# Kernel tuning notes

Hardware: AMD Instinct MI355X
Metric: run time of the kernel (lower is better)

The kernel has to match this reference:

```python
import jax, jax.numpy as jnp
import numpy as np

F, H1, H2, K, L = 16, 64, 64, 8, 8          # n_features, hidden sizes, num_bins, num_layers
NBP = 3 * K + 1                              # num_bijector_params per feature
RMIN, RMAX = -10.0, 10.0
MIN_BIN, MIN_SLOPE = 1e-4, 1e-4              # distrax RationalQuadraticSpline defaults


def setup_inputs() -> dict:
    key = jax.random.key(0)
    ks = jax.random.split(key, 11)
    B = 131072
    return {
        "x": jax.random.normal(ks[0], (B, F), jnp.float32),
        "W0": jax.random.normal(ks[1], (L, F, F), jnp.float32) * 0.1,
        "b0": jax.random.normal(ks[2], (L, F), jnp.float32) * 0.01,
        "W1": jax.random.normal(ks[3], (L, F, H1), jnp.float32) * 0.1,
        "b1": jax.random.normal(ks[4], (L, H1), jnp.float32) * 0.01,
        "W2": jax.random.normal(ks[5], (L, H1, H2), jnp.float32) * 0.1,
        "b2": jax.random.normal(ks[6], (L, H2), jnp.float32) * 0.01,
        "Wout": jax.random.normal(ks[7], (L, H2, F * NBP), jnp.float32) * 0.05,
        "bout": jax.random.normal(ks[8], (L, F * NBP), jnp.float32) * 0.01,
        # scalar-affine coupling params; scale kept positive (init is ones in the module)
        "scale": jnp.exp(0.05 * jax.random.normal(ks[9], (L, F), jnp.float32)),
        "shift": jax.random.normal(ks[10], (L, F), jnp.float32) * 0.1,
    }


def _rq_spline_fwd(params, x):
    """distrax.RationalQuadraticSpline forward_and_log_det (elementwise).
    params: (B, F, 3K+1), x: (B, F) -> (y, log_det) each (B, F)."""
    uw, uh, ud = params[..., :K], params[..., K:2 * K], params[..., 2 * K:]
    total = RMAX - RMIN
    w = jax.nn.softmax(uw, axis=-1) * (total - K * MIN_BIN) + MIN_BIN   # bin widths
    h = jax.nn.softmax(uh, axis=-1) * (total - K * MIN_BIN) + MIN_BIN   # bin heights
    offset = float(np.log(np.expm1(1.0 - MIN_SLOPE)))                   # softplus(0+offset)=1
    d = jax.nn.softplus(ud + offset) + MIN_SLOPE                        # knot slopes (B,F,K+1)
    zeros = jnp.zeros(w.shape[:-1] + (1,), w.dtype)
    xpos = RMIN + jnp.concatenate([zeros, jnp.cumsum(w, -1)], -1)       # knot x (B,F,K+1)
    ypos = RMIN + jnp.concatenate([zeros, jnp.cumsum(h, -1)], -1)       # knot y (B,F,K+1)
    # per-element bin search
    idx = jnp.clip(jnp.sum((x[..., None] >= xpos).astype(jnp.int32), -1) - 1, 0, K - 1)
    take = lambda a: jnp.take_along_axis(a, idx[..., None], axis=-1)[..., 0]
    xk, xk1 = take(xpos[..., :-1]), take(xpos[..., 1:])
    yk, yk1 = take(ypos[..., :-1]), take(ypos[..., 1:])
    dk, dk1 = take(d[..., :-1]), take(d[..., 1:])
    bw = xk1 - xk
    bh = yk1 - yk
    s = bh / bw                                                          # bin slope
    z = jnp.clip((x - xk) / bw, 0.0, 1.0)
    z1m = 1.0 - z
    den = s + (dk1 + dk - 2.0 * s) * z * z1m
    y = yk + bh * (s * z * z + dk * z * z1m) / den
    num_ld = dk1 * z * z + 2.0 * s * z * z1m + dk * z1m * z1m
    ld = 2.0 * jnp.log(s) + jnp.log(num_ld) - 2.0 * jnp.log(den)
    outside = (x <= RMIN) | (x >= RMAX)                                  # identity outside range
    return jnp.where(outside, x, y), jnp.where(outside, 0.0, ld)


def reference(x, W0, b0, W1, b1, W2, b2, Wout, bout, scale, shift):
    """log_prob of Transformed(base, Inverse(Chain(layers))) == base.log_prob(Chain.fwd(x)) + fwd logdet."""
    B = x.shape[0]
    feat = jnp.arange(F)
    z = x
    logdet = jnp.zeros((B,), x.dtype)
    # distrax.Chain applies the last-appended layer first -> iterate layers in reverse;
    # within layer i: spline coupling (appended second) then scalar-affine coupling.
    for i in reversed(range(L)):
        mask = ((feat + i) % 2).astype(bool)        # True = pass-through / conditioner input
        mz = jnp.where(mask, z, 0.0)
        hid = jnp.tanh(mz @ W0[i] + b0[i])
        hid = jnp.tanh(hid @ W1[i] + b1[i])
        hid = hid @ W2[i] + b2[i]                   # last MLP layer is linear
        p = (hid @ Wout[i] + bout[i]).reshape(B, F, NBP)
        y, ld = _rq_spline_fwd(p, z)
        z = jnp.where(mask, z, y)
        logdet = logdet + jnp.sum(jnp.where(mask, 0.0, ld), axis=-1)
        # scalar affine coupling with all-False mask: transforms every feature
        z = z * scale[i] + shift[i]
        logdet = logdet + jnp.sum(jnp.log(jnp.abs(scale[i])))
    base_lp = -0.5 * jnp.sum(z * z, axis=-1) - 0.5 * F * float(np.log(2.0 * np.pi))
    return base_lp + logdet
```

## Files before the change

### kernel.cpp

```cpp
#include <hip/hip_runtime.h>
#include <math.h>

typedef _Float16 f16;
typedef _Float16 half8 __attribute__((ext_vector_type(8)));
typedef float f32x16 __attribute__((ext_vector_type(16)));

#define DEV __device__ __forceinline__

#define W1F_OFF 0
#define W2F_OFF 16384
#define WOF_OFF 81920
#define BOF_OFF 344064
#define SUMLOG_OFF 352256
#define W0S_OFF 352320
#define B0S_OFF 360512
#define B1S_OFF 361088
#define BOT_OFF 363136

#define H0_OFF    0
#define H0_STRIDE 48
#define H_OFF     12288
#define H_STRIDE  144
#define P_OFF     49152
#define P_STRIDE  116
#define LDS_BYTES 78848

DEV float frcp(float x){ return __builtin_amdgcn_rcpf(x); }

#if __has_builtin(__builtin_amdgcn_exp2f)
DEV float fexp2(float x){ return __builtin_amdgcn_exp2f(x); }
#else
DEV float fexp2(float x){ return exp2f(x); }
#endif
#if __has_builtin(__builtin_amdgcn_logf)
DEV float flog2(float x){ return __builtin_amdgcn_logf(x); }
#else
DEV float flog2(float x){ return log2f(x); }
#endif

#define LN2F    0.69314718056f
#define LOG2EF  1.4426950409f
#define TWOLOG2EF 2.8853900818f

DEV float ftanh2(float x){
  float e = fexp2(x);
  float r = frcp(e + 1.f);
  return fmaf(-2.f, r, 1.f);
}

DEV void rq_spline(const float p[25], float xv, float &y_out, float &ld_out)
{
  float ew[8]; float sw = 0.f;
#pragma unroll
  for (int k = 0; k < 8; ++k){ ew[k] = fexp2(p[k]); sw += ew[k]; }
  float rw = frcp(sw) * 19.9992f;

  float xpos[9];
  xpos[0] = -10.f;
#pragma unroll
  for (int k = 0; k < 8; ++k) xpos[k + 1] = xpos[k] + fmaf(ew[k], rw, 1e-4f);

  bool b[8];
  int idx = 0;
#pragma unroll
  for (int j = 1; j < 8; ++j){ b[j] = (xv >= xpos[j]); idx += b[j] ? 1 : 0; }

  float xk = xpos[0], ewk = ew[0];
#pragma unroll
  for (int j = 1; j < 8; ++j){
    xk  = b[j] ? xpos[j] : xk;
    ewk = b[j] ? ew[j]   : ewk;
  }
  float bw = fmaf(ewk, rw, 1e-4f);

  float eh[8]; float shs = 0.f;
#pragma unroll
  for (int k = 0; k < 8; ++k){ eh[k] = fexp2(p[8 + k]); shs += eh[k]; }
  float rh = frcp(shs) * 19.9992f;

  float S = 0.f, ehk = eh[0];
#pragma unroll
  for (int k = 1; k < 8; ++k){
    S   += b[k] ? eh[k - 1] : 0.f;
    ehk  = b[k] ? eh[k]     : ehk;
  }
  float yk = fmaf(S, rh, fmaf((float)idx, 1e-4f, -10.f));
  float bh = fmaf(ehk, rh, 1e-4f);

  float vA = p[16], vB = p[17];
#pragma unroll
  for (int j = 1; j < 8; ++j){
    vA = b[j] ? p[16 + j] : vA;
    vB = b[j] ? p[17 + j] : vB;
  }
  float tA = fmaxf(vA, 0.f) + flog2(1.f + fexp2(-fabsf(vA)));
  float dk  = fmaf(LN2F, tA, 1e-4f);
  float tB = fmaxf(vB, 0.f) + flog2(1.f + fexp2(-fabsf(vB)));
  float dk1 = fmaf(LN2F, tB, 1e-4f);

  float rbw = frcp(bw);
  float s   = bh * rbw;
  float zf  = fminf(fmaxf((xv - xk) * rbw, 0.f), 1.f);
  float z1  = 1.f - zf;
  float zz  = zf * zf, z01 = zf * z1;
  float den = s + (dk1 + dk - 2.f * s) * z01;
  float rden = frcp(den);
  float yv  = yk + bh * (s * zz + dk * z01) * rden;
  float num = dk1 * zz + 2.f * s * z01 + dk * z1 * z1;
  float ldv2 = flog2(s * s * num * rden * rden);

  bool outside = (xv <= -10.f) || (xv >= 10.f);
  y_out  = outside ? xv : yv;
  ld_out = outside ? 0.f : ldv2;
}

extern "C" __global__ void __launch_bounds__(256)
prep_kernel(const float* __restrict__ W0, const float* __restrict__ b0,
            const float* __restrict__ W1, const float* __restrict__ b1,
            const float* __restrict__ W2,
            const float* __restrict__ Wo, const float* __restrict__ bout,
            const float* __restrict__ scale, char* __restrict__ ws)
{
  int tid = blockIdx.x * 256 + threadIdx.x;
  if (tid < 1024){
    int fi = tid >> 6, lane = tid & 63;
    int l = fi >> 1, nt = fi & 1;
    int n = nt * 32 + (lane & 31), khi = lane >> 5;
    half8 h;
#pragma unroll
    for (int j = 0; j < 8; ++j){ int k = khi * 8 + j; h[j] = (f16)(W1[l * 1024 + k * 64 + n] * TWOLOG2EF); }
    *(half8*)(ws + W1F_OFF + fi * 1024 + lane * 16) = h;
  } else if (tid < 5120){
    int idx = tid - 1024;
    int fi = idx >> 6, lane = idx & 63;
    int l = fi >> 3, kt = (fi >> 1) & 3, nt = fi & 1;
    int n = nt * 32 + (lane & 31), khi = lane >> 5;
    half8 h;
#pragma unroll
    for (int j = 0; j < 8; ++j){ int k = kt * 16 + khi * 8 + j; h[j] = (f16)W2[l * 4096 + k * 64 + n]; }
    *(half8*)(ws + W2F_OFF + fi * 1024 + lane * 16) = h;
  } else if (tid < 21504){
    int idx = tid - 5120;
    int fi = idx >> 6, lane = idx & 63;
    int l = fi >> 5, u = (fi >> 2) & 7, kt = fi & 3;
    int f = (l & 1) + 2 * u;
    int c = lane & 31, khi = lane >> 5;
    half8 h;
#pragma unroll
    for (int j = 0; j < 8; ++j){
      int k = kt * 16 + khi * 8 + j;
      float v = (c < 25) ? Wo[l * 25600 + k * 400 + f * 25 + c] * LOG2EF : 0.f;
      h[j] = (f16)v;
    }
    *(half8*)(ws + WOF_OFF + fi * 1024 + lane * 16) = h;
  } else if (tid < 23552){
    int idx = tid - 21504;
    int l = idx >> 8, u = (idx >> 5) & 7, c = idx & 31;
    int f = (l & 1) + 2 * u;
    float v = 0.f;
    if (c < 25){
      v = bout[l * 400 + f * 25 + c];
      if (c >= 16) v += 0.54116666f;
      v *= LOG2EF;
    }
    ((float*)(ws + BOF_OFF))[idx] = v;
  } else if (tid == 23552){
    float acc = 0.f;
    for (int i = 0; i < 128; ++i) acc += logf(fabsf(scale[i]));
    *(float*)(ws + SUMLOG_OFF) = acc;
  } else if (tid < 25601){
    int idx = tid - 23553;
    ((float*)(ws + W0S_OFF))[idx] = W0[idx] * TWOLOG2EF;
  } else if (tid < 25729){
    int idx = tid - 25601;
    ((float*)(ws + B0S_OFF))[idx] = b0[idx] * TWOLOG2EF;
  } else if (tid < 26241){
    int idx = tid - 25729;
    ((float*)(ws + B1S_OFF))[idx] = b1[idx] * TWOLOG2EF;
  } else if (tid < 28289){
    int idx = tid - 26241;
    int l = idx >> 8, u = (idx >> 5) & 7, kh = (idx >> 4) & 1, i = idx & 15;
    int f = (l & 1) + 2 * u;
    int r = (i & 3) + 8 * (i >> 2) + 4 * kh;
    float v = 0.f;
    if (r < 25){
      v = bout[l * 400 + f * 25 + r];
      if (r >= 16) v += 0.54116666f;
      v *= LOG2EF;
    }
    ((float*)(ws + BOT_OFF))[idx] = v;
  }
}

DEV void load_botv(const char* __restrict__ ws, int l, int u, int khi,
                   float (&botv)[16])
{
  const float4* bp = (const float4*)(ws + BOT_OFF) + ((l * 8 + u) * 2 + khi) * 4;
#pragma unroll
  for (int q = 0; q < 4; ++q){
    float4 v = bp[q];
    botv[q * 4]     = v.x;
    botv[q * 4 + 1] = v.y;
    botv[q * 4 + 2] = v.z;
    botv[q * 4 + 3] = v.w;
  }
}

DEV void wout_feature(const half8 (&a2)[2][4], const half8 (&bfn)[4],
                      const float (&botv)[16], char* lds,
                      int wv, int ln31, int khi)
{
  f32x16 dp[2];
#pragma unroll
  for (int mt = 0; mt < 2; ++mt)
#pragma unroll
    for (int i = 0; i < 16; ++i) dp[mt][i] = botv[i];
#pragma unroll
  for (int kt = 0; kt < 4; ++kt)
#pragma unroll
    for (int mt = 0; mt < 2; ++mt)
      dp[mt] = __builtin_amdgcn_mfma_f32_32x32x16_f16(bfn[kt], a2[mt][kt], dp[mt], 0, 0, 0);
#pragma unroll
  for (int mt = 0; mt < 2; ++mt){
    int s = wv * 64 + mt * 32 + ln31;
    char* base = lds + P_OFF + s * P_STRIDE + khi * 16;
#pragma unroll
    for (int i = 0; i < 12; ++i){
      int rc = (i & 3) + 8 * (i >> 2);
      *(float*)(base + rc * 4) = dp[mt][i];
    }
    if (khi == 0)
      *(float*)(base + 24 * 4) = dp[mt][12];
  }
}

template<int PAR>
DEV void layer_mfma(int l,
                    const float* __restrict__ b2v,
                    const float* __restrict__ scv, const float* __restrict__ shv,
                    const char* __restrict__ ws, char* lds,
                    float (&z)[16], float &logdet,
                    int t, int lane, int wv, int ln31, int khi)
{
  const float* w0  = (const float*)(ws + W0S_OFF) + l * 256;
  const float* bb0 = (const float*)(ws + B0S_OFF) + l * 16;
  const int rowbase = khi * 4;

  const half8* W1F = (const half8*)(ws + W1F_OFF);
  const half8* W2F = (const half8*)(ws + W2F_OFF);
  half8 w1f[2];
#pragma unroll
  for (int nt = 0; nt < 2; ++nt) w1f[nt] = W1F[(l * 2 + nt) * 64 + lane];
  half8 w2f[8];
#pragma unroll
  for (int kt = 0; kt < 4; ++kt)
#pragma unroll
    for (int nt = 0; nt < 2; ++nt)
      w2f[kt * 2 + nt] = W2F[((l * 4 + kt) * 2 + nt) * 64 + lane];
  float bias1[2], bias2[2];
#pragma unroll
  for (int nt = 0; nt < 2; ++nt){
    bias1[nt] = ((const float*)(ws + B1S_OFF))[l * 64 + nt * 32 + ln31];
    bias2[nt] = b2v[l * 64 + nt * 32 + ln31];
  }

  float h0[16];
#pragma unroll
  for (int j = 0; j < 16; ++j) h0[j] = bb0[j];
#pragma unroll
  for (int u = 0; u < 8; ++u){
    const int f = (1 - PAR) + 2 * u;
    const float v = z[f];
#pragma unroll
    for (int j = 0; j < 16; ++j) h0[j] = fmaf(v, w0[f * 16 + j], h0[j]);
  }
  {
    half8 lo, hi;
#pragma unroll
    for (int j = 0; j < 8; ++j){ lo[j] = (f16)ftanh2(h0[j]); hi[j] = (f16)ftanh2(h0[8 + j]); }
    *(half8*)(lds + H0_OFF + t * H0_STRIDE)      = lo;
    *(half8*)(lds + H0_OFF + t * H0_STRIDE + 16) = hi;
  }

  half8 a0[2];
#pragma unroll
  for (int mt = 0; mt < 2; ++mt){
    int s = wv * 64 + mt * 32 + ln31;
    a0[mt] = *(const half8*)(lds + H0_OFF + s * H0_STRIDE + khi * 16);
  }
  f32x16 d1[2][2];
#pragma unroll
  for (int mt = 0; mt < 2; ++mt)
#pragma unroll
    for (int nt = 0; nt < 2; ++nt)
#pragma unroll
      for (int i = 0; i < 16; ++i) d1[mt][nt][i] = bias1[nt];
#pragma unroll
  for (int nt = 0; nt < 2; ++nt)
#pragma unroll
    for (int mt = 0; mt < 2; ++mt)
      d1[mt][nt] = __builtin_amdgcn_mfma_f32_32x32x16_f16(a0[mt], w1f[nt], d1[mt][nt], 0, 0, 0);
#pragma unroll
  for (int mt = 0; mt < 2; ++mt)
#pragma unroll
    for (int nt = 0; nt < 2; ++nt)
#pragma unroll
      for (int i = 0; i < 16; ++i){
        int row = (i & 3) + 8 * (i >> 2) + rowbase;
        int s = wv * 64 + mt * 32 + row;
        float v = ftanh2(d1[mt][nt][i]);
        *(f16*)(lds + H_OFF + s * H_STRIDE + (nt * 32 + ln31) * 2) = (f16)v;
      }

  half8 a1[2][4];
#pragma unroll
  for (int mt = 0; mt < 2; ++mt){
    int s = wv * 64 + mt * 32 + ln31;
#pragma unroll
    for (int kt = 0; kt < 4; ++kt)
      a1[mt][kt] = *(const half8*)(lds + H_OFF + s * H_STRIDE + kt * 32 + khi * 16);
  }
  f32x16 d2[2][2];
#pragma unroll
  for (int mt = 0; mt < 2; ++mt)
#pragma unroll
    for (int nt = 0; nt < 2; ++nt)
#pragma unroll
      for (int i = 0; i < 16; ++i) d2[mt][nt][i] = bias2[nt];
#pragma unroll
  for (int kt = 0; kt < 4; ++kt)
#pragma unroll
    for (int nt = 0; nt < 2; ++nt)
#pragma unroll
      for (int mt = 0; mt < 2; ++mt)
        d2[mt][nt] = __builtin_amdgcn_mfma_f32_32x32x16_f16(a1[mt][kt], w2f[kt * 2 + nt], d2[mt][nt], 0, 0, 0);

  const half8* WOF = (const half8*)(ws + WOF_OFF);
  half8 bfn[4];
#pragma unroll
  for (int kt = 0; kt < 4; ++kt) bfn[kt] = WOF[((l * 8 + 0) * 4 + kt) * 64 + lane];
  float botv[16];
  load_botv(ws, l, 0, khi, botv);

#pragma unroll
  for (int mt = 0; mt < 2; ++mt)
#pragma unroll
    for (int nt = 0; nt < 2; ++nt)
#pragma unroll
      for (int i = 0; i < 16; ++i){
        int row = (i & 3) + 8 * (i >> 2) + rowbase;
        int s = wv * 64 + mt * 32 + row;
        float v = d2[mt][nt][i];
        *(f16*)(lds + H_OFF + s * H_STRIDE + (nt * 32 + ln31) * 2) = (f16)v;
      }

  half8 a2[2][4];
#pragma unroll
  for (int mt = 0; mt < 2; ++mt){
    int s = wv * 64 + mt * 32 + ln31;
#pragma unroll
    for (int kt = 0; kt < 4; ++kt)
      a2[mt][kt] = *(const half8*)(lds + H_OFF + s * H_STRIDE + kt * 32 + khi * 16);
  }

  wout_feature(a2, bfn, botv, lds, wv, ln31, khi);
#pragma unroll
  for (int kt = 0; kt < 4; ++kt) bfn[kt] = WOF[((l * 8 + 1) * 4 + kt) * 64 + lane];
  load_botv(ws, l, 1, khi, botv);

#pragma unroll 1
  for (int u = 0; u < 8; ++u){
    float p[25];
#pragma unroll
    for (int j = 0; j < 25; ++j)
      p[j] = *(const float*)(lds + P_OFF + t * P_STRIDE + j * 4);

    if (u < 7){
      wout_feature(a2, bfn, botv, lds, wv, ln31, khi);
      if (u < 6){
#pragma unroll
        for (int kt = 0; kt < 4; ++kt) bfn[kt] = WOF[((l * 8 + u + 2) * 4 + kt) * 64 + lane];
        load_botv(ws, l, u + 2, khi, botv);
      }
    }

    const int f = PAR + 2 * u;
    float y, ld;
    rq_spline(p, z[f], y, ld);
    z[f] = y;
    logdet += ld;
  }

  const float* scp = scv + l * 16;
  const float* shp = shv + l * 16;
#pragma unroll
  for (int j = 0; j < 16; ++j)
    z[j] = fmaf(z[j], scp[j], shp[j]);
}

extern "C" __global__ void __launch_bounds__(256, 2)
flow_kernel(const float* __restrict__ x,
            const float* __restrict__ b2v,
            const float* __restrict__ scv, const float* __restrict__ shv,
            const char* __restrict__ ws, float* __restrict__ out, int B)
{
  extern __shared__ char lds[];
  const int t    = threadIdx.x;
  const int lane = t & 63;
  const int wv   = t >> 6;
  const int ln31 = lane & 31;
  const int khi  = lane >> 5;
  const int g    = blockIdx.x * 256 + t;

  float z[16];
  const float4* xv = reinterpret_cast<const float4*>(x + (size_t)g * 16);
  float4 a0 = xv[0], a1 = xv[1], a2 = xv[2], a3 = xv[3];
  z[0]=a0.x; z[1]=a0.y; z[2]=a0.z; z[3]=a0.w;
  z[4]=a1.x; z[5]=a1.y; z[6]=a1.z; z[7]=a1.w;
  z[8]=a2.x; z[9]=a2.y; z[10]=a2.z; z[11]=a2.w;
  z[12]=a3.x; z[13]=a3.y; z[14]=a3.z; z[15]=a3.w;

  float logdet = 0.f;
  for (int l = 7; l >= 0; --l){
    if (l & 1) layer_mfma<1>(l, b2v, scv, shv, ws, lds, z, logdet, t, lane, wv, ln31, khi);
    else       layer_mfma<0>(l, b2v, scv, shv, ws, lds, z, logdet, t, lane, wv, ln31, khi);
  }

  float sumlog = *(const float*)(ws + SUMLOG_OFF);
  float ss = 0.f;
#pragma unroll
  for (int j = 0; j < 16; ++j) ss = fmaf(z[j], z[j], ss);
  out[g] = fmaf(LN2F, logdet, -0.5f * ss - 14.7030165f + sumlog);
}

extern "C" void kernel_launch(void* const* d_in, const int* in_sizes, int n_in,
                              void* d_out, int out_size, void* d_ws, size_t ws_size,
                              hipStream_t stream)
{
  const float* x    = (const float*)d_in[0];
  const float* W0   = (const float*)d_in[1];
  const float* b0   = (const float*)d_in[2];
  const float* W1   = (const float*)d_in[3];
  const float* b1   = (const float*)d_in[4];
  const float* W2   = (const float*)d_in[5];
  const float* b2   = (const float*)d_in[6];
  const float* Wout = (const float*)d_in[7];
  const float* bout = (const float*)d_in[8];
  const float* scale= (const float*)d_in[9];
  const float* shift= (const float*)d_in[10];

  int B = in_sizes[0] / 16;

  hipLaunchKernelGGL(prep_kernel, dim3(111), dim3(256), 0, stream,
                     W0, b0, W1, b1, W2, Wout, bout, scale, (char*)d_ws);

  hipLaunchKernelGGL(flow_kernel, dim3(B / 256), dim3(256), LDS_BYTES, stream,
                     x, b2, scale, shift,
                     (const char*)d_ws, (float*)d_out, B);
}
```

Before: 192.0 us.

## Transpose hidden MFMAs, alias per-wave LDS arena, raise occupancy to three blocks

Swaps the MFMA operand order for the two hidden layers so outputs come out transposed, which lets tanh results be written to LDS as packed half4 stores instead of scalar f16 stores. Biases are pre-laid out in the transposed accumulator order by the prep kernel. The H0, H and P buffers are aliased inside one 12 KB per-wave arena, shrinking LDS from about 77 KB to 48 KB, and launch bounds are raised to three blocks per CU. The aim is fewer LDS store instructions and higher occupancy. The cost is tighter register pressure under the new launch bound and reliance on wave-private LDS reuse, which is only safe because each wave touches nothing but its own arena.

```diff
diff --git a/kernel.cpp b/kernel.cpp
--- a/kernel.cpp
+++ b/kernel.cpp
@@ -2,7 +2,9 @@
 #include <math.h>
 
 typedef _Float16 f16;
+typedef _Float16 half4 __attribute__((ext_vector_type(4)));
 typedef _Float16 half8 __attribute__((ext_vector_type(8)));
+typedef float f32x4  __attribute__((ext_vector_type(4)));
 typedef float f32x16 __attribute__((ext_vector_type(16)));
 
 #define DEV __device__ __forceinline__
@@ -10,7 +12,8 @@
 #define W1F_OFF 0
 #define W2F_OFF 16384
 #define WOF_OFF 81920
-#define BOF_OFF 344064
+#define B1T_OFF 344064
+#define B2T_OFF 346112
 #define SUMLOG_OFF 352256
 #define W0S_OFF 352320
 #define B0S_OFF 360512
@@ -19,11 +22,12 @@
 
 #define H0_OFF    0
 #define H0_STRIDE 48
-#define H_OFF     12288
+#define H_OFF     3072
 #define H_STRIDE  144
-#define P_OFF     49152
+#define P_OFF     0
 #define P_STRIDE  116
-#define LDS_BYTES 78848
+#define ARENA     12288
+#define LDS_BYTES (4 * ARENA)
 
 DEV float frcp(float x){ return __builtin_amdgcn_rcpf(x); }
 
@@ -117,7 +121,7 @@
 extern "C" __global__ void __launch_bounds__(256)
 prep_kernel(const float* __restrict__ W0, const float* __restrict__ b0,
             const float* __restrict__ W1, const float* __restrict__ b1,
-            const float* __restrict__ W2,
+            const float* __restrict__ W2, const float* __restrict__ b2,
             const float* __restrict__ Wo, const float* __restrict__ bout,
             const float* __restrict__ scale, char* __restrict__ ws)
 {
@@ -153,31 +157,27 @@
       h[j] = (f16)v;
     }
     *(half8*)(ws + WOF_OFF + fi * 1024 + lane * 16) = h;
-  } else if (tid < 23552){
+  } else if (tid < 22016){
     int idx = tid - 21504;
-    int l = idx >> 8, u = (idx >> 5) & 7, c = idx & 31;
-    int f = (l & 1) + 2 * u;
-    float v = 0.f;
-    if (c < 25){
-      v = bout[l * 400 + f * 25 + c];
-      if (c >= 16) v += 0.54116666f;
-      v *= LOG2EF;
-    }
-    ((float*)(ws + BOF_OFF))[idx] = v;
+    int l = idx >> 6, nt = (idx >> 5) & 1, kh = (idx >> 4) & 1, i = idx & 15;
+    int r = (i & 3) + 8 * (i >> 2) + 4 * kh;
+    ((float*)(ws + B1T_OFF))[idx] = b1[l * 64 + nt * 32 + r] * TWOLOG2EF;
+  } else if (tid < 22528){
+    int idx = tid - 22016;
+    int l = idx >> 6, nt = (idx >> 5) & 1, kh = (idx >> 4) & 1, i = idx & 15;
+    int r = (i & 3) + 8 * (i >> 2) + 4 * kh;
+    ((float*)(ws + B2T_OFF))[idx] = b2[l * 64 + nt * 32 + r];
   } else if (tid == 23552){
     float acc = 0.f;
     for (int i = 0; i < 128; ++i) acc += logf(fabsf(scale[i]));
     *(float*)(ws + SUMLOG_OFF) = acc;
-  } else if (tid < 25601){
+  } else if (tid > 23552 && tid < 25601){
     int idx = tid - 23553;
     ((float*)(ws + W0S_OFF))[idx] = W0[idx] * TWOLOG2EF;
-  } else if (tid < 25729){
+  } else if (tid >= 25601 && tid < 25729){
     int idx = tid - 25601;
     ((float*)(ws + B0S_OFF))[idx] = b0[idx] * TWOLOG2EF;
-  } else if (tid < 26241){
-    int idx = tid - 25729;
-    ((float*)(ws + B1S_OFF))[idx] = b1[idx] * TWOLOG2EF;
-  } else if (tid < 28289){
+  } else if (tid >= 26241 && tid < 28289){
     int idx = tid - 26241;
     int l = idx >> 8, u = (idx >> 5) & 7, kh = (idx >> 4) & 1, i = idx & 15;
     int f = (l & 1) + 2 * u;
@@ -195,20 +195,16 @@
 DEV void load_botv(const char* __restrict__ ws, int l, int u, int khi,
                    float (&botv)[16])
 {
-  const float4* bp = (const float4*)(ws + BOT_OFF) + ((l * 8 + u) * 2 + khi) * 4;
-#pragma unroll
-  for (int q = 0; q < 4; ++q){
-    float4 v = bp[q];
-    botv[q * 4]     = v.x;
-    botv[q * 4 + 1] = v.y;
-    botv[q * 4 + 2] = v.z;
-    botv[q * 4 + 3] = v.w;
+  const f32x4* bp = (const f32x4*)(ws + BOT_OFF) + ((l * 8 + u) * 2 + khi) * 4;
+  f32x4 q0 = bp[0], q1 = bp[1], q2 = bp[2], q3 = bp[3];
+#pragma unroll
+  for (int i = 0; i < 4; ++i){
+    botv[i] = q0[i]; botv[4 + i] = q1[i]; botv[8 + i] = q2[i]; botv[12 + i] = q3[i];
   }
 }
 
 DEV void wout_feature(const half8 (&a2)[2][4], const half8 (&bfn)[4],
-                      const float (&botv)[16], char* lds,
-                      int wv, int ln31, int khi)
+                      const float (&botv)[16], char* ldsw, int ln31, int khi)
 {
   f32x16 dp[2];
 #pragma unroll
@@ -222,29 +218,27 @@
       dp[mt] = __builtin_amdgcn_mfma_f32_32x32x16_f16(bfn[kt], a2[mt][kt], dp[mt], 0, 0, 0);
 #pragma unroll
   for (int mt = 0; mt < 2; ++mt){
-    int s = wv * 64 + mt * 32 + ln31;
-    char* base = lds + P_OFF + s * P_STRIDE + khi * 16;
+    int s = mt * 32 + ln31;
+    char* base = ldsw + P_OFF + s * P_STRIDE + khi * 16;
 #pragma unroll
     for (int i = 0; i < 12; ++i){
       int rc = (i & 3) + 8 * (i >> 2);
       *(float*)(base + rc * 4) = dp[mt][i];
     }
     if (khi == 0)
-      *(float*)(base + 24 * 4) = dp[mt][12];
+      *(float*)(base + 96) = dp[mt][12];
   }
 }
 
 template<int PAR>
 DEV void layer_mfma(int l,
-                    const float* __restrict__ b2v,
                     const float* __restrict__ scv, const float* __restrict__ shv,
-                    const char* __restrict__ ws, char* lds,
+                    const char* __restrict__ ws, char* ldsw,
                     float (&z)[16], float &logdet,
-                    int t, int lane, int wv, int ln31, int khi)
+                    int lane, int ln31, int khi)
 {
   const float* w0  = (const float*)(ws + W0S_OFF) + l * 256;
   const float* bb0 = (const float*)(ws + B0S_OFF) + l * 16;
-  const int rowbase = khi * 4;
 
   const half8* W1F = (const half8*)(ws + W1F_OFF);
   const half8* W2F = (const half8*)(ws + W2F_OFF);
@@ -257,12 +251,6 @@
 #pragma unroll
     for (int nt = 0; nt < 2; ++nt)
       w2f[kt * 2 + nt] = W2F[((l * 4 + kt) * 2 + nt) * 64 + lane];
-  float bias1[2], bias2[2];
-#pragma unroll
-  for (int nt = 0; nt < 2; ++nt){
-    bias1[nt] = ((const float*)(ws + B1S_OFF))[l * 64 + nt * 32 + ln31];
-    bias2[nt] = b2v[l * 64 + nt * 32 + ln31];
-  }
 
   float h0[16];
 #pragma unroll
@@ -278,62 +266,78 @@
     half8 lo, hi;
 #pragma unroll
     for (int j = 0; j < 8; ++j){ lo[j] = (f16)ftanh2(h0[j]); hi[j] = (f16)ftanh2(h0[8 + j]); }
-    *(half8*)(lds + H0_OFF + t * H0_STRIDE)      = lo;
-    *(half8*)(lds + H0_OFF + t * H0_STRIDE + 16) = hi;
+    *(half8*)(ldsw + H0_OFF + lane * H0_STRIDE)      = lo;
+    *(half8*)(ldsw + H0_OFF + lane * H0_STRIDE + 16) = hi;
   }
 
   half8 a0[2];
 #pragma unroll
-  for (int mt = 0; mt < 2; ++mt){
-    int s = wv * 64 + mt * 32 + ln31;
-    a0[mt] = *(const half8*)(lds + H0_OFF + s * H0_STRIDE + khi * 16);
-  }
-  f32x16 d1[2][2];
-#pragma unroll
   for (int mt = 0; mt < 2; ++mt)
+    a0[mt] = *(const half8*)(ldsw + H0_OFF + (mt * 32 + ln31) * H0_STRIDE + khi * 16);
+  f32x16 d1t[2][2];
+  {
+    const f32x4* B1T = (const f32x4*)(ws + B1T_OFF);
+#pragma unroll
+    for (int nt = 0; nt < 2; ++nt){
+      const f32x4* bp = B1T + ((l * 2 + nt) * 2 + khi) * 4;
+      f32x4 q0 = bp[0], q1 = bp[1], q2 = bp[2], q3 = bp[3];
+#pragma unroll
+      for (int mt = 0; mt < 2; ++mt)
+#pragma unroll
+        for (int i = 0; i < 4; ++i){
+          d1t[nt][mt][i] = q0[i]; d1t[nt][mt][4 + i] = q1[i];
+          d1t[nt][mt][8 + i] = q2[i]; d1t[nt][mt][12 + i] = q3[i];
+        }
+    }
+  }
+#pragma unroll
+  for (int nt = 0; nt < 2; ++nt)
+#pragma unroll
+    for (int mt = 0; mt < 2; ++mt)
+      d1t[nt][mt] = __builtin_amdgcn_mfma_f32_32x32x16_f16(w1f[nt], a0[mt], d1t[nt][mt], 0, 0, 0);
+#pragma unroll
+  for (int nt = 0; nt < 2; ++nt)
+#pragma unroll
+    for (int mt = 0; mt < 2; ++mt){
+      int s = mt * 32 + ln31;
+#pragma unroll
+      for (int g = 0; g < 4; ++g){
+        half4 h4;
+#pragma unroll
+        for (int j = 0; j < 4; ++j) h4[j] = (f16)ftanh2(d1t[nt][mt][g * 4 + j]);
+        *(half4*)(ldsw + H_OFF + s * H_STRIDE + nt * 64 + g * 16 + khi * 8) = h4;
+      }
+    }
+
+  half8 a1[2][4];
+#pragma unroll
+  for (int mt = 0; mt < 2; ++mt)
+#pragma unroll
+    for (int kt = 0; kt < 4; ++kt)
+      a1[mt][kt] = *(const half8*)(ldsw + H_OFF + (mt * 32 + ln31) * H_STRIDE + kt * 32 + khi * 16);
+  f32x16 d2t[2][2];
+  {
+    const f32x4* B2T = (const f32x4*)(ws + B2T_OFF);
+#pragma unroll
+    for (int nt = 0; nt < 2; ++nt){
+      const f32x4* bp = B2T + ((l * 2 + nt) * 2 + khi) * 4;
+      f32x4 q0 = bp[0], q1 = bp[1], q2 = bp[2], q3 = bp[3];
+#pragma unroll
+      for (int mt = 0; mt < 2; ++mt)
+#pragma unroll
+        for (int i = 0; i < 4; ++i){
+          d2t[nt][mt][i] = q0[i]; d2t[nt][mt][4 + i] = q1[i];
+          d2t[nt][mt][8 + i] = q2[i]; d2t[nt][mt][12 + i] = q3[i];
+        }
+    }
+  }
+#pragma unroll
+  for (int kt = 0; kt < 4; ++kt)
 #pragma unroll
     for (int nt = 0; nt < 2; ++nt)
 #pragma unroll
-      for (int i = 0; i < 16; ++i) d1[mt][nt][i] = bias1[nt];
-#pragma unroll
-  for (int nt = 0; nt < 2; ++nt)
-#pragma unroll
-    for (int mt = 0; mt < 2; ++mt)
-      d1[mt][nt] = __builtin_amdgcn_mfma_f32_32x32x16_f16(a0[mt], w1f[nt], d1[mt][nt], 0, 0, 0);
-#pragma unroll
-  for (int mt = 0; mt < 2; ++mt)
-#pragma unroll
-    for (int nt = 0; nt < 2; ++nt)
-#pragma unroll
-      for (int i = 0; i < 16; ++i){
-        int row = (i & 3) + 8 * (i >> 2) + rowbase;
-        int s = wv * 64 + mt * 32 + row;
-        float v = ftanh2(d1[mt][nt][i]);
-        *(f16*)(lds + H_OFF + s * H_STRIDE + (nt * 32 + ln31) * 2) = (f16)v;
-      }
-
-  half8 a1[2][4];
-#pragma unroll
-  for (int mt = 0; mt < 2; ++mt){
-    int s = wv * 64 + mt * 32 + ln31;
-#pragma unroll
-    for (int kt = 0; kt < 4; ++kt)
-      a1[mt][kt] = *(const half8*)(lds + H_OFF + s * H_STRIDE + kt * 32 + khi * 16);
-  }
-  f32x16 d2[2][2];
-#pragma unroll
-  for (int mt = 0; mt < 2; ++mt)
-#pragma unroll
-    for (int nt = 0; nt < 2; ++nt)
-#pragma unroll
-      for (int i = 0; i < 16; ++i) d2[mt][nt][i] = bias2[nt];
-#pragma unroll
-  for (int kt = 0; kt < 4; ++kt)
-#pragma unroll
-    for (int nt = 0; nt < 2; ++nt)
-#pragma unroll
       for (int mt = 0; mt < 2; ++mt)
-        d2[mt][nt] = __builtin_amdgcn_mfma_f32_32x32x16_f16(a1[mt][kt], w2f[kt * 2 + nt], d2[mt][nt], 0, 0, 0);
+        d2t[nt][mt] = __builtin_amdgcn_mfma_f32_32x32x16_f16(w2f[kt * 2 + nt], a1[mt][kt], d2t[nt][mt], 0, 0, 0);
 
   const half8* WOF = (const half8*)(ws + WOF_OFF);
   half8 bfn[4];
@@ -343,27 +347,27 @@
   load_botv(ws, l, 0, khi, botv);
 
 #pragma unroll
+  for (int nt = 0; nt < 2; ++nt)
+#pragma unroll
+    for (int mt = 0; mt < 2; ++mt){
+      int s = mt * 32 + ln31;
+#pragma unroll
+      for (int g = 0; g < 4; ++g){
+        half4 h4;
+#pragma unroll
+        for (int j = 0; j < 4; ++j) h4[j] = (f16)d2t[nt][mt][g * 4 + j];
+        *(half4*)(ldsw + H_OFF + s * H_STRIDE + nt * 64 + g * 16 + khi * 8) = h4;
+      }
+    }
+
+  half8 a2[2][4];
+#pragma unroll
   for (int mt = 0; mt < 2; ++mt)
 #pragma unroll
-    for (int nt = 0; nt < 2; ++nt)
-#pragma unroll
-      for (int i = 0; i < 16; ++i){
-        int row = (i & 3) + 8 * (i >> 2) + rowbase;
-        int s = wv * 64 + mt * 32 + row;
-        float v = d2[mt][nt][i];
-        *(f16*)(lds + H_OFF + s * H_STRIDE + (nt * 32 + ln31) * 2) = (f16)v;
-      }
-
-  half8 a2[2][4];
-#pragma unroll
-  for (int mt = 0; mt < 2; ++mt){
-    int s = wv * 64 + mt * 32 + ln31;
-#pragma unroll
     for (int kt = 0; kt < 4; ++kt)
-      a2[mt][kt] = *(const half8*)(lds + H_OFF + s * H_STRIDE + kt * 32 + khi * 16);
-  }
-
-  wout_feature(a2, bfn, botv, lds, wv, ln31, khi);
+      a2[mt][kt] = *(const half8*)(ldsw + H_OFF + (mt * 32 + ln31) * H_STRIDE + kt * 32 + khi * 16);
+
+  wout_feature(a2, bfn, botv, ldsw, ln31, khi);
 #pragma unroll
   for (int kt = 0; kt < 4; ++kt) bfn[kt] = WOF[((l * 8 + 1) * 4 + kt) * 64 + lane];
   load_botv(ws, l, 1, khi, botv);
@@ -373,10 +377,10 @@
     float p[25];
 #pragma unroll
     for (int j = 0; j < 25; ++j)
-      p[j] = *(const float*)(lds + P_OFF + t * P_STRIDE + j * 4);
+      p[j] = *(const float*)(ldsw + P_OFF + lane * P_STRIDE + j * 4);
 
     if (u < 7){
-      wout_feature(a2, bfn, botv, lds, wv, ln31, khi);
+      wout_feature(a2, bfn, botv, ldsw, ln31, khi);
       if (u < 6){
 #pragma unroll
         for (int kt = 0; kt < 4; ++kt) bfn[kt] = WOF[((l * 8 + u + 2) * 4 + kt) * 64 + lane];
@@ -398,9 +402,8 @@
     z[j] = fmaf(z[j], scp[j], shp[j]);
 }
 
-extern "C" __global__ void __launch_bounds__(256, 2)
+extern "C" __global__ void __launch_bounds__(256, 3)
 flow_kernel(const float* __restrict__ x,
-            const float* __restrict__ b2v,
             const float* __restrict__ scv, const float* __restrict__ shv,
             const char* __restrict__ ws, float* __restrict__ out, int B)
 {
@@ -410,7 +413,8 @@
   const int wv   = t >> 6;
   const int ln31 = lane & 31;
   const int khi  = lane >> 5;
-  const int g    = blockIdx.x * 256 + t;
+  char* ldsw = lds + wv * ARENA;
+  const int g = blockIdx.x * 256 + t;
 
   float z[16];
   const float4* xv = reinterpret_cast<const float4*>(x + (size_t)g * 16);
@@ -422,8 +426,8 @@
 
   float logdet = 0.f;
   for (int l = 7; l >= 0; --l){
-    if (l & 1) layer_mfma<1>(l, b2v, scv, shv, ws, lds, z, logdet, t, lane, wv, ln31, khi);
-    else       layer_mfma<0>(l, b2v, scv, shv, ws, lds, z, logdet, t, lane, wv, ln31, khi);
+    if (l & 1) layer_mfma<1>(l, scv, shv, ws, ldsw, z, logdet, lane, ln31, khi);
+    else       layer_mfma<0>(l, scv, shv, ws, ldsw, z, logdet, lane, ln31, khi);
   }
 
   float sumlog = *(const float*)(ws + SUMLOG_OFF);
@@ -452,9 +456,9 @@
   int B = in_sizes[0] / 16;
 
   hipLaunchKernelGGL(prep_kernel, dim3(111), dim3(256), 0, stream,
-                     W0, b0, W1, b1, W2, Wout, bout, scale, (char*)d_ws);
+                     W0, b0, W1, b1, W2, b2, Wout, bout, scale, (char*)d_ws);
 
   hipLaunchKernelGGL(flow_kernel, dim3(B / 256), dim3(256), LDS_BYTES, stream,
-                     x, b2, scale, shift,
+                     x, scale, shift,
                      (const char*)d_ws, (float*)d_out, B);
 }
```

After: 198.9 us. 3.6% more time.
